# Optimization experiments

Hardware: AMD Instinct MI355X
Metric: run time of the kernel (lower is better)

Reference implementation:

```python
import jax, jax.numpy as jnp
import numpy as np

D_MODEL = 1024
N_HEAD = 16
D_HEAD = D_MODEL // N_HEAD
NEG = -1e9


def setup_inputs() -> dict:
    key = jax.random.key(0)
    ks = jax.random.split(key, 11)
    B, T, C = 4, 2048, D_MODEL
    s = 1.0 / np.sqrt(C)
    return {
        "q": jax.random.normal(ks[0], (B, T, C), jnp.float32),
        "k": jax.random.normal(ks[1], (B, T, C), jnp.float32),
        "v": jax.random.normal(ks[2], (B, T, C), jnp.float32),
        "w_q": jax.random.normal(ks[3], (C, C), jnp.float32) * s,
        "b_q": jnp.zeros((C,), jnp.float32),
        "w_k": jax.random.normal(ks[4], (C, C), jnp.float32) * s,
        "b_k": jnp.zeros((C,), jnp.float32),
        "w_v": jax.random.normal(ks[5], (C, C), jnp.float32) * s,
        "b_v": jnp.zeros((C,), jnp.float32),
        "w_o": jax.random.normal(ks[6], (C, C), jnp.float32) * s,
        "b_o": jnp.zeros((C,), jnp.float32),
    }


def reference(q, k, v, w_q, b_q, w_k, b_k, w_v, b_v, w_o, b_o):
    B, T, C = q.shape
    # projections; weights stored as [in, out]
    qh = (q @ w_q + b_q).reshape(B, T, N_HEAD, D_HEAD).transpose(0, 2, 1, 3)
    kh = (k @ w_k + b_k).reshape(B, T, N_HEAD, D_HEAD).transpose(0, 2, 1, 3)
    vh = (v @ w_v + b_v).reshape(B, T, N_HEAD, D_HEAD).transpose(0, 2, 1, 3)
    scores = jnp.einsum("bhqd,bhkd->bhqk", qh, kh) / jnp.sqrt(
        jnp.asarray(D_HEAD, qh.dtype))
    causal = jnp.tril(jnp.ones((T, T), dtype=bool))  # [T,T]
    scores = jnp.where(causal[None, None], scores, NEG)
    attn = jax.nn.softmax(scores, axis=-1)
    out = jnp.einsum("bhqk,bhkd->bhqd", attn, vh)
    out = out.transpose(0, 2, 1, 3).reshape(B, T, C)
    return out @ w_o + b_o
```

## Files before the change

### kernel.cpp

```cpp
#include <hip/hip_runtime.h>
#include <hip/hip_bf16.h>
#include <cstdint>
#include <cstddef>

#define DEVI static __device__ __forceinline__

typedef __attribute__((ext_vector_type(8))) short short8;
typedef __attribute__((ext_vector_type(4))) float f32x4;

typedef __attribute__((address_space(1))) const unsigned int as1c_uint;
typedef __attribute__((address_space(3))) unsigned int as3_uint;

constexpr int Bn = 4, Tn = 2048, Cn = 1024, Hn = 16, Dn = 64;
constexpr int Mtot = Bn * Tn;
#define QSCALE (0.125f * 1.44269504088896340736f)

DEVI unsigned short f2bf(float f) {
  unsigned u = __float_as_uint(f);
  u += 0x7fffu + ((u >> 16) & 1u);
  return (unsigned short)(u >> 16);
}
DEVI unsigned short f2bf_t(float f) {
  return (unsigned short)(__float_as_uint(f) >> 16);
}

DEVI void async16(const void* g, void* l) {
  __builtin_amdgcn_global_load_lds((as1c_uint*)g, (as3_uint*)l, 16, 0, 0);
}

__global__ __launch_bounds__(256) void cvt3_kernel(
    const float4* __restrict__ i0, const float4* __restrict__ i1,
    const float4* __restrict__ i2, ushort4* __restrict__ o0,
    ushort4* __restrict__ o1, ushort4* __restrict__ o2, int n4, int zoff) {
  const int z = blockIdx.y + zoff;
  const float4* in = z == 0 ? i0 : z == 1 ? i1 : i2;
  ushort4* out = z == 0 ? o0 : z == 1 ? o1 : o2;
  const int stride = gridDim.x * blockDim.x;
  for (int i = blockIdx.x * blockDim.x + threadIdx.x; i < n4; i += stride) {
    float4 v = in[i];
    ushort4 o;
    o.x = f2bf(v.x); o.y = f2bf(v.y); o.z = f2bf(v.z); o.w = f2bf(v.w);
    out[i] = o;
  }
}

__global__ __launch_bounds__(256) void transpose_cvt4(
    const float* __restrict__ w0, const float* __restrict__ w1,
    const float* __restrict__ w2, const float* __restrict__ w3,
    unsigned short* __restrict__ o0, unsigned short* __restrict__ o1,
    unsigned short* __restrict__ o2, unsigned short* __restrict__ o3) {
  __shared__ float tile[32][33];
  const int z = blockIdx.z;
  const float* w = z == 0 ? w0 : z == 1 ? w1 : z == 2 ? w2 : w3;
  unsigned short* wT = z == 0 ? o0 : z == 1 ? o1 : z == 2 ? o2 : o3;
  int n0 = blockIdx.x * 32, k0 = blockIdx.y * 32;
  int tx = threadIdx.x, ty = threadIdx.y;
#pragma unroll
  for (int r = 0; r < 32; r += 8)
    tile[ty + r][tx] = w[(size_t)(k0 + ty + r) * Cn + n0 + tx];
  __syncthreads();
  const int t = ty * 32 + tx;
  const int n_l = t >> 3;
  const int kq = (t & 7) * 4;
  const int n = n0 + n_l, k = k0 + kq;
  ushort4 pk;
#pragma unroll
  for (int e = 0; e < 4; ++e) ((unsigned short*)&pk)[e] = f2bf(tile[kq + e][n_l]);
  size_t idx = (size_t)((((n >> 4) * 32 + (k >> 5)) * 64 + ((k >> 3) & 3) * 16 + (n & 15))) * 8 + (k & 7);
  *(ushort4*)&wT[idx] = pk;
}

DEVI short8 xfrag(const unsigned short* Xlds, int i, int kc, int l15, int l4) {
  int row = i * 16 + l15;
  return *(const short8*)&Xlds[row * 1024 + (((kc * 4 + l4) ^ (row & 7)) * 8)];
}

template <int NJ, bool SWAP>
DEVI void proj_core(const unsigned short* __restrict__ wF,
                    const unsigned short* Xlds, int njb, int lane,
                    f32x4 (&acc)[4][NJ]) {
  const int l15 = lane & 15, l4 = lane >> 4;
  const short8* wp = (const short8*)wF;
  short8 wfA[NJ], wfB[NJ];
#pragma unroll
  for (int j = 0; j < NJ; ++j) wfA[j] = wp[((njb + j) * 32) * 64 + lane];
#pragma unroll 1
  for (int kc = 0; kc < 32; kc += 2) {
#pragma unroll
    for (int j = 0; j < NJ; ++j) wfB[j] = wp[((njb + j) * 32 + kc + 1) * 64 + lane];
    short8 xf[4];
#pragma unroll
    for (int i = 0; i < 4; ++i) xf[i] = xfrag(Xlds, i, kc, l15, l4);
#pragma unroll
    for (int i = 0; i < 4; ++i)
#pragma unroll
      for (int j = 0; j < NJ; ++j)
        acc[i][j] = SWAP
            ? __builtin_amdgcn_mfma_f32_16x16x32_bf16(xf[i], wfA[j], acc[i][j], 0, 0, 0)
            : __builtin_amdgcn_mfma_f32_16x16x32_bf16(wfA[j], xf[i], acc[i][j], 0, 0, 0);
    if (kc + 2 < 32) {
#pragma unroll
      for (int j = 0; j < NJ; ++j) wfA[j] = wp[((njb + j) * 32 + kc + 2) * 64 + lane];
    }
#pragma unroll
    for (int i = 0; i < 4; ++i) xf[i] = xfrag(Xlds, i, kc + 1, l15, l4);
#pragma unroll
    for (int i = 0; i < 4; ++i)
#pragma unroll
      for (int j = 0; j < NJ; ++j)
        acc[i][j] = SWAP
            ? __builtin_amdgcn_mfma_f32_16x16x32_bf16(xf[i], wfB[j], acc[i][j], 0, 0, 0)
            : __builtin_amdgcn_mfma_f32_16x16x32_bf16(wfB[j], xf[i], acc[i][j], 0, 0, 0);
  }
}

DEVI void stage_strip(const unsigned short* __restrict__ src, int m0,
                      unsigned short* Xlds, int tid) {
#pragma unroll
  for (int it = 0; it < 16; ++it) {
    int s = it * 512 + tid;
    int row = s >> 7, sl = s & 127;
    async16(src + (size_t)(m0 + row) * Cn + ((sl ^ (row & 7)) * 8),
            Xlds + (size_t)(it * 512 + (tid & ~63)) * 8);
  }
}

__global__ __launch_bounds__(512, 2) void proj_qkv(
    const unsigned short* __restrict__ xq, const unsigned short* __restrict__ xk,
    const unsigned short* __restrict__ xv, const unsigned short* __restrict__ wFq,
    const unsigned short* __restrict__ wFk, const unsigned short* __restrict__ wFv,
    const float* __restrict__ bq, const float* __restrict__ bk,
    const float* __restrict__ bv, unsigned short* __restrict__ oq,
    unsigned short* __restrict__ ok, unsigned short* __restrict__ ov, int zoff) {
  __shared__ unsigned short Xlds[64 * 1024];
  const int tid = threadIdx.x, lane = tid & 63, w = tid >> 6;
  const int l15 = lane & 15, l4 = lane >> 4;
  const int bid = blockIdx.x;
  const int z = zoff + (bid >> 7);
  const int m0 = (bid & 127) * 64;
  const unsigned short* xz = z == 0 ? xq : z == 1 ? xk : xv;
  const unsigned short* wF = z == 0 ? wFq : z == 1 ? wFk : wFv;
  const float* bias = z == 0 ? bq : z == 1 ? bk : bv;

  stage_strip(xz, m0, Xlds, tid);
  __syncthreads();

  const f32x4 zf = {0.f, 0.f, 0.f, 0.f};
  f32x4 acc[4][8];
#pragma unroll
  for (int i = 0; i < 4; ++i)
#pragma unroll
    for (int j = 0; j < 8; ++j) acc[i][j] = zf;

  const int njb = w * 8;
  if (z < 2)
    proj_core<8, false>(wF, Xlds, njb, lane, acc);
  else
    proj_core<8, true>(wF, Xlds, njb, lane, acc);

  const int b = m0 >> 11, t0loc = m0 & 2047;
  if (z < 2) {
    unsigned short* o = z == 0 ? oq : ok;
    const float scale = z == 0 ? QSCALE : 1.f;
#pragma unroll
    for (int j = 0; j < 8; ++j) {
      int ng = njb + j;
      int h = ng >> 2, d0 = (ng & 3) * 16 + l4 * 4;
      float4 bv4 = *(const float4*)&bias[ng * 16 + l4 * 4];
#pragma unroll
      for (int i = 0; i < 4; ++i) {
        int t = t0loc + i * 16 + l15;
        ushort4 pk;
        pk.x = f2bf((acc[i][j][0] + bv4.x) * scale);
        pk.y = f2bf((acc[i][j][1] + bv4.y) * scale);
        pk.z = f2bf((acc[i][j][2] + bv4.z) * scale);
        pk.w = f2bf((acc[i][j][3] + bv4.w) * scale);
        *(ushort4*)&o[((size_t)((b * Hn + h) * Tn + t)) * Dn + d0] = pk;
      }
    }
  } else {
#pragma unroll
    for (int j = 0; j < 8; ++j) {
      int n = (njb + j) * 16 + l15;
      int h = n >> 6, d = n & 63;
      float bvl = bias[n];
#pragma unroll
      for (int i = 0; i < 4; ++i) {
        int t0 = t0loc + i * 16 + l4 * 4;
        ushort4 pk;
        pk.x = f2bf(acc[i][j][0] + bvl);
        pk.y = f2bf(acc[i][j][1] + bvl);
        pk.z = f2bf(acc[i][j][2] + bvl);
        pk.w = f2bf(acc[i][j][3] + bvl);
        *(ushort4*)&ov[((size_t)((b * Hn + h) * Dn + d)) * Tn + t0] = pk;
      }
    }
  }
}

__global__ __launch_bounds__(512, 2) void proj_out(
    const unsigned short* __restrict__ A, const unsigned short* __restrict__ wFo,
    const float* __restrict__ bias, float* __restrict__ o) {
  __shared__ unsigned short Xlds[64 * 1024];
  const int tid = threadIdx.x, lane = tid & 63, w = tid >> 6;
  const int l15 = lane & 15, l4 = lane >> 4;
  const int bid = blockIdx.x;
  const int m0 = (bid >> 1) * 64, nh = bid & 1;

  stage_strip(A, m0, Xlds, tid);
  __syncthreads();

  const f32x4 zf = {0.f, 0.f, 0.f, 0.f};
  f32x4 acc[4][4];
#pragma unroll
  for (int i = 0; i < 4; ++i)
#pragma unroll
    for (int j = 0; j < 4; ++j) acc[i][j] = zf;

  const int njb = nh * 32 + w * 4;
  proj_core<4, false>(wFo, Xlds, njb, lane, acc);

#pragma unroll
  for (int j = 0; j < 4; ++j) {
    int ng = njb + j;
    float4 bv4 = *(const float4*)&bias[ng * 16 + l4 * 4];
#pragma unroll
    for (int i = 0; i < 4; ++i) {
      int m = m0 + i * 16 + l15;
      float4 ov4;
      ov4.x = acc[i][j][0] + bv4.x;
      ov4.y = acc[i][j][1] + bv4.y;
      ov4.z = acc[i][j][2] + bv4.z;
      ov4.w = acc[i][j][3] + bv4.w;
      *(float4*)&o[(size_t)m * Cn + ng * 16 + l4 * 4] = ov4;
    }
  }
}

__global__ __launch_bounds__(512) void attn_kernel(const unsigned short* __restrict__ qh,
                                                   const unsigned short* __restrict__ kh,
                                                   const unsigned short* __restrict__ vt,
                                                   unsigned short* __restrict__ obf) {
  __shared__ unsigned short Ks[2][64 * 64];
  __shared__ unsigned short Vs[2][64 * 64];
  __shared__ unsigned short Ps[8][16 * 72];

  const int tid = threadIdx.x, lane = tid & 63, w = tid >> 6;
  const int l15 = lane & 15, l4 = lane >> 4;
  const int swz = l15 & 7;

  const int bid = blockIdx.x;
  const int j = bid >> 3;
  const int bh = (bid & 7) * 8 + (j & 7);
  const int pair = j >> 3;
  const unsigned short* qb = qh + (size_t)bh * Tn * Dn;
  const unsigned short* kb = kh + (size_t)bh * Tn * Dn;
  const unsigned short* vb = vt + (size_t)bh * Dn * Tn;
  const int b = bh >> 4, h = bh & 15;

  const int srow = lane >> 3, sslot = (lane & 7) ^ (lane >> 3);

  const f32x4 z = {0.f, 0.f, 0.f, 0.f};
  const short ob = (short)0x3F80;
  const short8 ones = {ob, ob, ob, ob, ob, ob, ob, ob};

#pragma unroll 1
  for (int half = 0; half < 2; ++half) {
    const int qt = half == 0 ? pair : 15 - pair;
    const int q0 = qt * 128;
    const int qrow = q0 + w * 16 + l15;

    short8 qf0 = *(const short8*)(qb + (size_t)qrow * Dn + l4 * 8);
    short8 qf1 = *(const short8*)(qb + (size_t)qrow * Dn + 32 + l4 * 8);

    f32x4 o[4];
#pragma unroll
    for (int nd = 0; nd < 4; ++nd) o[nd] = z;
    f32x4 osum = z;

    const int nt = (q0 >> 6) + 2;
    const int ntw = ((q0 + w * 16 + 15) >> 6) + 1;

    {
      const unsigned short* ksrc = kb + (size_t)(w * 8 + srow) * Dn + sslot * 8;
      const unsigned short* vsrc = vb + (size_t)(w * 8 + srow) * Tn + sslot * 8;
      async16(ksrc, &Ks[0][w * 512]);
      async16(vsrc, &Vs[0][w * 512]);
    }

#pragma unroll 1
    for (int t = 0; t < nt; ++t) {
      const int cur = t & 1;
      if (t + 1 < nt) {
        const int kv1 = (t + 1) * 64;
        const unsigned short* ksrc = kb + (size_t)(kv1 + w * 8 + srow) * Dn + sslot * 8;
        const unsigned short* vsrc = vb + (size_t)(w * 8 + srow) * Tn + kv1 + sslot * 8;
        async16(ksrc, &Ks[cur ^ 1][w * 512]);
        async16(vsrc, &Vs[cur ^ 1][w * 512]);
        asm volatile("s_waitcnt vmcnt(2)" ::: "memory");
      } else {
        asm volatile("s_waitcnt vmcnt(0)" ::: "memory");
      }
      __builtin_amdgcn_s_barrier();
      __builtin_amdgcn_sched_barrier(0);

      if (t < ntw) {
        const unsigned short* Kc = &Ks[cur][0];
        const unsigned short* Vc = &Vs[cur][0];

        f32x4 s[4];
#pragma unroll
        for (int ni = 0; ni < 4; ++ni) s[ni] = z;
        __builtin_amdgcn_s_setprio(1);
#pragma unroll
        for (int ni = 0; ni < 4; ++ni) {
          const int rb = (ni * 16 + l15) * 64;
          short8 kf0 = *(const short8*)&Kc[rb + ((l4 ^ swz) * 8)];
          short8 kf1 = *(const short8*)&Kc[rb + (((4 + l4) ^ swz) * 8)];
          s[ni] = __builtin_amdgcn_mfma_f32_16x16x32_bf16(kf0, qf0, s[ni], 0, 0, 0);
          s[ni] = __builtin_amdgcn_mfma_f32_16x16x32_bf16(kf1, qf1, s[ni], 0, 0, 0);
        }
        __builtin_amdgcn_s_setprio(0);

        short8 vf[8];
#pragma unroll
        for (int nd = 0; nd < 4; ++nd) {
          const int rb = (nd * 16 + l15) * 64;
          vf[nd * 2]     = *(const short8*)&Vc[rb + ((l4 ^ swz) * 8)];
          vf[nd * 2 + 1] = *(const short8*)&Vc[rb + (((4 + l4) ^ swz) * 8)];
        }

        const int kq = qrow - t * 64;
        const bool edge = (t * 64 + 63 > q0 + w * 16);
        if (!edge) {
#pragma unroll
          for (int ni = 0; ni < 4; ++ni) {
            ushort4 pk;
#pragma unroll
            for (int r = 0; r < 4; ++r)
              ((unsigned short*)&pk)[r] = f2bf_t(__builtin_amdgcn_exp2f(s[ni][r]));
            *(ushort4*)&Ps[w][l15 * 72 + ni * 16 + l4 * 4] = pk;
          }
        } else {
#pragma unroll
          for (int ni = 0; ni < 4; ++ni) {
            ushort4 pk;
#pragma unroll
            for (int r = 0; r < 4; ++r) {
              float e = __builtin_amdgcn_exp2f(s[ni][r]);
              if ((ni * 16 + l4 * 4 + r) > kq) e = 0.f;
              ((unsigned short*)&pk)[r] = f2bf_t(e);
            }
            *(ushort4*)&Ps[w][l15 * 72 + ni * 16 + l4 * 4] = pk;
          }
        }
        asm volatile("s_waitcnt lgkmcnt(0)" ::: "memory");
        __builtin_amdgcn_sched_barrier(0);

        short8 pf0 = *(const short8*)&Ps[w][l15 * 72 + l4 * 8];
        short8 pf1 = *(const short8*)&Ps[w][l15 * 72 + 32 + l4 * 8];
        __builtin_amdgcn_s_setprio(1);
        osum = __builtin_amdgcn_mfma_f32_16x16x32_bf16(pf0, ones, osum, 0, 0, 0);
        osum = __builtin_amdgcn_mfma_f32_16x16x32_bf16(pf1, ones, osum, 0, 0, 0);
#pragma unroll
        for (int nd = 0; nd < 4; ++nd) {
          o[nd] = __builtin_amdgcn_mfma_f32_16x16x32_bf16(pf0, vf[nd * 2], o[nd], 0, 0, 0);
          o[nd] = __builtin_amdgcn_mfma_f32_16x16x32_bf16(pf1, vf[nd * 2 + 1], o[nd], 0, 0, 0);
        }
        __builtin_amdgcn_s_setprio(0);
      }

      __builtin_amdgcn_sched_barrier(0);
      __builtin_amdgcn_s_barrier();
    }

#pragma unroll
    for (int r = 0; r < 4; ++r) {
      float inv = __builtin_amdgcn_rcpf(osum[r]);
      int tq = q0 + w * 16 + l4 * 4 + r;
      size_t base = ((size_t)(b * Tn + tq)) * Cn + h * 64;
#pragma unroll
      for (int nd = 0; nd < 4; ++nd)
        obf[base + nd * 16 + l15] = f2bf(o[nd][r] * inv);
    }
  }
}

extern "C" void kernel_launch(void* const* d_in, const int* in_sizes, int n_in,
                              void* d_out, int out_size, void* d_ws, size_t ws_size,
                              hipStream_t stream) {
  const float* q   = (const float*)d_in[0];
  const float* k   = (const float*)d_in[1];
  const float* v   = (const float*)d_in[2];
  const float* w_q = (const float*)d_in[3];
  const float* b_q = (const float*)d_in[4];
  const float* w_k = (const float*)d_in[5];
  const float* b_k = (const float*)d_in[6];
  const float* w_v = (const float*)d_in[7];
  const float* b_v = (const float*)d_in[8];
  const float* w_o = (const float*)d_in[9];
  const float* b_o = (const float*)d_in[10];

  char* ws = (char*)d_ws;
  const size_t MB = 1u << 20;
  const bool big = ws_size >= 104 * MB;
  const int n4 = Mtot * Cn / 4;

  unsigned short *xq, *xk, *xv, *qhp, *khp, *vtp, *wqT, *wkT, *wvT, *woT;
  if (big) {
    xq  = (unsigned short*)(ws);
    xk  = (unsigned short*)(ws + 16 * MB);
    xv  = (unsigned short*)(ws + 32 * MB);
    qhp = (unsigned short*)(ws + 48 * MB);
    khp = (unsigned short*)(ws + 64 * MB);
    vtp = (unsigned short*)(ws + 80 * MB);
    wqT = (unsigned short*)(ws + 96 * MB);
    wkT = (unsigned short*)(ws + 98 * MB);
    wvT = (unsigned short*)(ws + 100 * MB);
    woT = (unsigned short*)(ws + 102 * MB);
  } else {
    xq = xk = xv = (unsigned short*)(ws);
    wqT = (unsigned short*)(ws + 16 * MB);
    wkT = (unsigned short*)(ws + 18 * MB);
    wvT = (unsigned short*)(ws + 20 * MB);
    woT = (unsigned short*)(ws + 22 * MB);
    qhp = (unsigned short*)(ws + 24 * MB);
    khp = (unsigned short*)(ws + 40 * MB);
    vtp = (unsigned short*)(ws + 56 * MB);
  }
  unsigned short* aout = xq;

  transpose_cvt4<<<dim3(32, 32, 4), dim3(32, 8), 0, stream>>>(
      w_q, w_k, w_v, w_o, wqT, wkT, wvT, woT);

  if (big) {
    cvt3_kernel<<<dim3(2048, 3), 256, 0, stream>>>(
        (const float4*)q, (const float4*)k, (const float4*)v,
        (ushort4*)xq, (ushort4*)xk, (ushort4*)xv, n4, 0);
    proj_qkv<<<384, 512, 0, stream>>>(xq, xk, xv, wqT, wkT, wvT,
                                      b_q, b_k, b_v, qhp, khp, vtp, 0);
  } else {
    for (int z = 0; z < 3; ++z) {
      cvt3_kernel<<<dim3(2048, 1), 256, 0, stream>>>(
          (const float4*)q, (const float4*)k, (const float4*)v,
          (ushort4*)xq, (ushort4*)xq, (ushort4*)xq, n4, z);
      proj_qkv<<<128, 512, 0, stream>>>(xq, xq, xq, wqT, wkT, wvT,
                                        b_q, b_k, b_v, qhp, khp, vtp, z);
    }
  }

  attn_kernel<<<512, 512, 0, stream>>>(qhp, khp, vtp, aout);

  proj_out<<<256, 512, 0, stream>>>(aout, woT, b_o, (float*)d_out);
}
```

Measured before the change: 181.2 us.

## Fuse fp32-to-bf16 input conversion into projection staging and halve row tiles

Drops the separate conversion kernel. The QKV projection now reads fp32 activations directly, converts them to bf16 and writes them into swizzled LDS, which removes one full write and read of the activations through HBM. Both projection kernels switch to 32-row strips with half the LDS, doubling the grid and raising the occupancy target to 4 blocks per CU. Each weight fragment is now reused over fewer rows, so weight traffic per FLOP goes up, and the staging path changes from async LDS loads to synchronous register loads.

```diff
diff --git a/kernel.cpp b/kernel.cpp
--- a/kernel.cpp
+++ b/kernel.cpp
@@ -26,22 +26,6 @@
 
 DEVI void async16(const void* g, void* l) {
   __builtin_amdgcn_global_load_lds((as1c_uint*)g, (as3_uint*)l, 16, 0, 0);
-}
-
-__global__ __launch_bounds__(256) void cvt3_kernel(
-    const float4* __restrict__ i0, const float4* __restrict__ i1,
-    const float4* __restrict__ i2, ushort4* __restrict__ o0,
-    ushort4* __restrict__ o1, ushort4* __restrict__ o2, int n4, int zoff) {
-  const int z = blockIdx.y + zoff;
-  const float4* in = z == 0 ? i0 : z == 1 ? i1 : i2;
-  ushort4* out = z == 0 ? o0 : z == 1 ? o1 : o2;
-  const int stride = gridDim.x * blockDim.x;
-  for (int i = blockIdx.x * blockDim.x + threadIdx.x; i < n4; i += stride) {
-    float4 v = in[i];
-    ushort4 o;
-    o.x = f2bf(v.x); o.y = f2bf(v.y); o.z = f2bf(v.z); o.w = f2bf(v.w);
-    out[i] = o;
-  }
 }
 
 __global__ __launch_bounds__(256) void transpose_cvt4(
@@ -75,49 +59,67 @@
   return *(const short8*)&Xlds[row * 1024 + (((kc * 4 + l4) ^ (row & 7)) * 8)];
 }
 
-template <int NJ, bool SWAP>
+template <int IB, int NJ, bool SWAP>
 DEVI void proj_core(const unsigned short* __restrict__ wF,
                     const unsigned short* Xlds, int njb, int lane,
-                    f32x4 (&acc)[4][NJ]) {
+                    f32x4 (&acc)[IB][NJ]) {
   const int l15 = lane & 15, l4 = lane >> 4;
+  constexpr int H = NJ / 2;
   const short8* wp = (const short8*)wF;
-  short8 wfA[NJ], wfB[NJ];
-#pragma unroll
-  for (int j = 0; j < NJ; ++j) wfA[j] = wp[((njb + j) * 32) * 64 + lane];
+  short8 wfc[H], wfn[H];
+#pragma unroll
+  for (int h = 0; h < H; ++h) wfc[h] = wp[(size_t)((njb + h) * 32) * 64 + lane];
 #pragma unroll 1
-  for (int kc = 0; kc < 32; kc += 2) {
-#pragma unroll
-    for (int j = 0; j < NJ; ++j) wfB[j] = wp[((njb + j) * 32 + kc + 1) * 64 + lane];
-    short8 xf[4];
-#pragma unroll
-    for (int i = 0; i < 4; ++i) xf[i] = xfrag(Xlds, i, kc, l15, l4);
-#pragma unroll
-    for (int i = 0; i < 4; ++i)
-#pragma unroll
-      for (int j = 0; j < NJ; ++j)
-        acc[i][j] = SWAP
-            ? __builtin_amdgcn_mfma_f32_16x16x32_bf16(xf[i], wfA[j], acc[i][j], 0, 0, 0)
-            : __builtin_amdgcn_mfma_f32_16x16x32_bf16(wfA[j], xf[i], acc[i][j], 0, 0, 0);
-    if (kc + 2 < 32) {
-#pragma unroll
-      for (int j = 0; j < NJ; ++j) wfA[j] = wp[((njb + j) * 32 + kc + 2) * 64 + lane];
-    }
-#pragma unroll
-    for (int i = 0; i < 4; ++i) xf[i] = xfrag(Xlds, i, kc + 1, l15, l4);
-#pragma unroll
-    for (int i = 0; i < 4; ++i)
-#pragma unroll
-      for (int j = 0; j < NJ; ++j)
-        acc[i][j] = SWAP
-            ? __builtin_amdgcn_mfma_f32_16x16x32_bf16(xf[i], wfB[j], acc[i][j], 0, 0, 0)
-            : __builtin_amdgcn_mfma_f32_16x16x32_bf16(wfB[j], xf[i], acc[i][j], 0, 0, 0);
-  }
-}
-
-DEVI void stage_strip(const unsigned short* __restrict__ src, int m0,
+  for (int kc = 0; kc < 32; ++kc) {
+#pragma unroll
+    for (int h = 0; h < H; ++h)
+      wfn[h] = wp[(size_t)((njb + H + h) * 32 + kc) * 64 + lane];
+    short8 xf[IB];
+#pragma unroll
+    for (int i = 0; i < IB; ++i) xf[i] = xfrag(Xlds, i, kc, l15, l4);
+#pragma unroll
+    for (int i = 0; i < IB; ++i)
+#pragma unroll
+      for (int h = 0; h < H; ++h)
+        acc[i][h] = SWAP
+            ? __builtin_amdgcn_mfma_f32_16x16x32_bf16(xf[i], wfc[h], acc[i][h], 0, 0, 0)
+            : __builtin_amdgcn_mfma_f32_16x16x32_bf16(wfc[h], xf[i], acc[i][h], 0, 0, 0);
+    if (kc + 1 < 32) {
+#pragma unroll
+      for (int h = 0; h < H; ++h)
+        wfc[h] = wp[(size_t)((njb + h) * 32 + kc + 1) * 64 + lane];
+    }
+#pragma unroll
+    for (int i = 0; i < IB; ++i)
+#pragma unroll
+      for (int h = 0; h < H; ++h)
+        acc[i][H + h] = SWAP
+            ? __builtin_amdgcn_mfma_f32_16x16x32_bf16(xf[i], wfn[h], acc[i][H + h], 0, 0, 0)
+            : __builtin_amdgcn_mfma_f32_16x16x32_bf16(wfn[h], xf[i], acc[i][H + h], 0, 0, 0);
+  }
+}
+
+DEVI void stage32_f32(const float* __restrict__ src, int m0,
                       unsigned short* Xlds, int tid) {
 #pragma unroll
-  for (int it = 0; it < 16; ++it) {
+  for (int it = 0; it < 8; ++it) {
+    int g = it * 512 + tid;
+    int row = g >> 7, slot = g & 127;
+    const float4* p = (const float4*)(src + (size_t)(m0 + row) * Cn + slot * 8);
+    float4 a = p[0], b = p[1];
+    short8 sv;
+    sv[0] = (short)f2bf(a.x); sv[1] = (short)f2bf(a.y);
+    sv[2] = (short)f2bf(a.z); sv[3] = (short)f2bf(a.w);
+    sv[4] = (short)f2bf(b.x); sv[5] = (short)f2bf(b.y);
+    sv[6] = (short)f2bf(b.z); sv[7] = (short)f2bf(b.w);
+    *(short8*)&Xlds[row * 1024 + ((slot ^ (row & 7)) * 8)] = sv;
+  }
+}
+
+DEVI void stage32_bf(const unsigned short* __restrict__ src, int m0,
+                     unsigned short* Xlds, int tid) {
+#pragma unroll
+  for (int it = 0; it < 8; ++it) {
     int s = it * 512 + tid;
     int row = s >> 7, sl = s & 127;
     async16(src + (size_t)(m0 + row) * Cn + ((sl ^ (row & 7)) * 8),
@@ -125,38 +127,38 @@
   }
 }
 
-__global__ __launch_bounds__(512, 2) void proj_qkv(
-    const unsigned short* __restrict__ xq, const unsigned short* __restrict__ xk,
-    const unsigned short* __restrict__ xv, const unsigned short* __restrict__ wFq,
+__global__ __launch_bounds__(512, 4) void proj_qkv(
+    const float* __restrict__ xqf, const float* __restrict__ xkf,
+    const float* __restrict__ xvf, const unsigned short* __restrict__ wFq,
     const unsigned short* __restrict__ wFk, const unsigned short* __restrict__ wFv,
     const float* __restrict__ bq, const float* __restrict__ bk,
     const float* __restrict__ bv, unsigned short* __restrict__ oq,
-    unsigned short* __restrict__ ok, unsigned short* __restrict__ ov, int zoff) {
-  __shared__ unsigned short Xlds[64 * 1024];
+    unsigned short* __restrict__ ok, unsigned short* __restrict__ ov) {
+  __shared__ unsigned short Xlds[32 * 1024];
   const int tid = threadIdx.x, lane = tid & 63, w = tid >> 6;
   const int l15 = lane & 15, l4 = lane >> 4;
   const int bid = blockIdx.x;
-  const int z = zoff + (bid >> 7);
-  const int m0 = (bid & 127) * 64;
-  const unsigned short* xz = z == 0 ? xq : z == 1 ? xk : xv;
+  const int z = bid >> 8;
+  const int m0 = (bid & 255) * 32;
+  const float* xz = z == 0 ? xqf : z == 1 ? xkf : xvf;
   const unsigned short* wF = z == 0 ? wFq : z == 1 ? wFk : wFv;
   const float* bias = z == 0 ? bq : z == 1 ? bk : bv;
 
-  stage_strip(xz, m0, Xlds, tid);
+  stage32_f32(xz, m0, Xlds, tid);
   __syncthreads();
 
   const f32x4 zf = {0.f, 0.f, 0.f, 0.f};
-  f32x4 acc[4][8];
-#pragma unroll
-  for (int i = 0; i < 4; ++i)
+  f32x4 acc[2][8];
+#pragma unroll
+  for (int i = 0; i < 2; ++i)
 #pragma unroll
     for (int j = 0; j < 8; ++j) acc[i][j] = zf;
 
   const int njb = w * 8;
   if (z < 2)
-    proj_core<8, false>(wF, Xlds, njb, lane, acc);
+    proj_core<2, 8, false>(wF, Xlds, njb, lane, acc);
   else
-    proj_core<8, true>(wF, Xlds, njb, lane, acc);
+    proj_core<2, 8, true>(wF, Xlds, njb, lane, acc);
 
   const int b = m0 >> 11, t0loc = m0 & 2047;
   if (z < 2) {
@@ -168,7 +170,7 @@
       int h = ng >> 2, d0 = (ng & 3) * 16 + l4 * 4;
       float4 bv4 = *(const float4*)&bias[ng * 16 + l4 * 4];
 #pragma unroll
-      for (int i = 0; i < 4; ++i) {
+      for (int i = 0; i < 2; ++i) {
         int t = t0loc + i * 16 + l15;
         ushort4 pk;
         pk.x = f2bf((acc[i][j][0] + bv4.x) * scale);
@@ -185,7 +187,7 @@
       int h = n >> 6, d = n & 63;
       float bvl = bias[n];
 #pragma unroll
-      for (int i = 0; i < 4; ++i) {
+      for (int i = 0; i < 2; ++i) {
         int t0 = t0loc + i * 16 + l4 * 4;
         ushort4 pk;
         pk.x = f2bf(acc[i][j][0] + bvl);
@@ -198,34 +200,34 @@
   }
 }
 
-__global__ __launch_bounds__(512, 2) void proj_out(
+__global__ __launch_bounds__(512, 4) void proj_out(
     const unsigned short* __restrict__ A, const unsigned short* __restrict__ wFo,
     const float* __restrict__ bias, float* __restrict__ o) {
-  __shared__ unsigned short Xlds[64 * 1024];
+  __shared__ unsigned short Xlds[32 * 1024];
   const int tid = threadIdx.x, lane = tid & 63, w = tid >> 6;
   const int l15 = lane & 15, l4 = lane >> 4;
   const int bid = blockIdx.x;
-  const int m0 = (bid >> 1) * 64, nh = bid & 1;
-
-  stage_strip(A, m0, Xlds, tid);
+  const int m0 = (bid >> 1) * 32, nh = bid & 1;
+
+  stage32_bf(A, m0, Xlds, tid);
   __syncthreads();
 
   const f32x4 zf = {0.f, 0.f, 0.f, 0.f};
-  f32x4 acc[4][4];
-#pragma unroll
-  for (int i = 0; i < 4; ++i)
+  f32x4 acc[2][4];
+#pragma unroll
+  for (int i = 0; i < 2; ++i)
 #pragma unroll
     for (int j = 0; j < 4; ++j) acc[i][j] = zf;
 
   const int njb = nh * 32 + w * 4;
-  proj_core<4, false>(wFo, Xlds, njb, lane, acc);
+  proj_core<2, 4, false>(wFo, Xlds, njb, lane, acc);
 
 #pragma unroll
   for (int j = 0; j < 4; ++j) {
     int ng = njb + j;
     float4 bv4 = *(const float4*)&bias[ng * 16 + l4 * 4];
 #pragma unroll
-    for (int i = 0; i < 4; ++i) {
+    for (int i = 0; i < 2; ++i) {
       int m = m0 + i * 16 + l15;
       float4 ov4;
       ov4.x = acc[i][j][0] + bv4.x;
@@ -403,53 +405,22 @@
 
   char* ws = (char*)d_ws;
   const size_t MB = 1u << 20;
-  const bool big = ws_size >= 104 * MB;
-  const int n4 = Mtot * Cn / 4;
-
-  unsigned short *xq, *xk, *xv, *qhp, *khp, *vtp, *wqT, *wkT, *wvT, *woT;
-  if (big) {
-    xq  = (unsigned short*)(ws);
-    xk  = (unsigned short*)(ws + 16 * MB);
-    xv  = (unsigned short*)(ws + 32 * MB);
-    qhp = (unsigned short*)(ws + 48 * MB);
-    khp = (unsigned short*)(ws + 64 * MB);
-    vtp = (unsigned short*)(ws + 80 * MB);
-    wqT = (unsigned short*)(ws + 96 * MB);
-    wkT = (unsigned short*)(ws + 98 * MB);
-    wvT = (unsigned short*)(ws + 100 * MB);
-    woT = (unsigned short*)(ws + 102 * MB);
-  } else {
-    xq = xk = xv = (unsigned short*)(ws);
-    wqT = (unsigned short*)(ws + 16 * MB);
-    wkT = (unsigned short*)(ws + 18 * MB);
-    wvT = (unsigned short*)(ws + 20 * MB);
-    woT = (unsigned short*)(ws + 22 * MB);
-    qhp = (unsigned short*)(ws + 24 * MB);
-    khp = (unsigned short*)(ws + 40 * MB);
-    vtp = (unsigned short*)(ws + 56 * MB);
-  }
-  unsigned short* aout = xq;
+  unsigned short* qhp  = (unsigned short*)(ws);
+  unsigned short* khp  = (unsigned short*)(ws + 16 * MB);
+  unsigned short* vtp  = (unsigned short*)(ws + 32 * MB);
+  unsigned short* aout = (unsigned short*)(ws + 48 * MB);
+  unsigned short* wqT  = (unsigned short*)(ws + 64 * MB);
+  unsigned short* wkT  = (unsigned short*)(ws + 66 * MB);
+  unsigned short* wvT  = (unsigned short*)(ws + 68 * MB);
+  unsigned short* woT  = (unsigned short*)(ws + 70 * MB);
 
   transpose_cvt4<<<dim3(32, 32, 4), dim3(32, 8), 0, stream>>>(
       w_q, w_k, w_v, w_o, wqT, wkT, wvT, woT);
 
-  if (big) {
-    cvt3_kernel<<<dim3(2048, 3), 256, 0, stream>>>(
-        (const float4*)q, (const float4*)k, (const float4*)v,
-        (ushort4*)xq, (ushort4*)xk, (ushort4*)xv, n4, 0);
-    proj_qkv<<<384, 512, 0, stream>>>(xq, xk, xv, wqT, wkT, wvT,
-                                      b_q, b_k, b_v, qhp, khp, vtp, 0);
-  } else {
-    for (int z = 0; z < 3; ++z) {
-      cvt3_kernel<<<dim3(2048, 1), 256, 0, stream>>>(
-          (const float4*)q, (const float4*)k, (const float4*)v,
-          (ushort4*)xq, (ushort4*)xq, (ushort4*)xq, n4, z);
-      proj_qkv<<<128, 512, 0, stream>>>(xq, xq, xq, wqT, wkT, wvT,
-                                        b_q, b_k, b_v, qhp, khp, vtp, z);
-    }
-  }
+  proj_qkv<<<768, 512, 0, stream>>>(q, k, v, wqT, wkT, wvT,
+                                    b_q, b_k, b_v, qhp, khp, vtp);
 
   attn_kernel<<<512, 512, 0, stream>>>(qhp, khp, vtp, aout);
 
-  proj_out<<<256, 512, 0, stream>>>(aout, woT, b_o, (float*)d_out);
-}
+  proj_out<<<512, 512, 0, stream>>>(aout, woT, b_o, (float*)d_out);
+}
```

After: 172.3 us. -4.9%, faster.
